# Kernel tuning notes

Measured on AMD Instinct MI355X. Metric: run time of the kernel, lower is better.

## Reference

```python
import jax, jax.numpy as jnp
import numpy as np

K = 8              # kernel_size
C_IN = 3           # input_channels
HID = 256          # hidden_state_size
MID = 256          # mid_layer_size
N_MAIN = 4         # num_main_layers
N_CLS = 1000       # num_classes
N_PIX = K * K      # num_pixel_values
IN_VEC = 2 + 1 + N_PIX * C_IN + HID   # 451
OUT_VEC = 2 + 1 + HID                 # 259
B, H, W = 128, 256, 256


def _lin_init(k, fan_in, fan_out):
    kw, kb = jax.random.split(k)
    bound = 1.0 / np.sqrt(fan_in)
    w = jax.random.uniform(kw, (fan_in, fan_out), jnp.float32, -bound, bound)
    b = jax.random.uniform(kb, (fan_out,), jnp.float32, -bound, bound)
    return w, b


def setup_inputs() -> dict:
    key = jax.random.key(0)
    ks = jax.random.split(key, 16)
    image = jax.random.normal(ks[0], (B, C_IN, H, W), jnp.float32)
    locations = jax.random.uniform(ks[1], (B, 2), jnp.float32)
    scales = jax.random.uniform(ks[2], (B, 1), jnp.float32)
    hidden_state = jax.random.normal(ks[3], (B, HID), jnp.float32)
    w0, b0 = _lin_init(ks[4], IN_VEC, MID)
    rws, rbs = [], []
    for i in range(N_MAIN):
        w, b = _lin_init(jax.random.fold_in(ks[5], i), MID, MID)
        rws.append(w); rbs.append(b)
    rw = jnp.stack(rws); rb = jnp.stack(rbs)          # [4,MID,MID], [4,MID]
    wf, bf = _lin_init(ks[6], MID, OUT_VEC)
    cw0, cb0 = _lin_init(ks[7], HID, MID)
    crw, crb = _lin_init(ks[8], MID, MID)
    cw1, cb1 = _lin_init(ks[9], MID, N_CLS)
    return {"image": image, "locations": locations, "scales": scales,
            "hidden_state": hidden_state, "w0": w0, "b0": b0, "rw": rw,
            "rb": rb, "wf": wf, "bf": bf, "cw0": cw0, "cb0": cb0,
            "crw": crw, "crb": crb, "cw1": cw1, "cb1": cb1}


def fourier_interp_2d(image, sample_points):
    """Band-limited (NUDFT) interpolation of image at continuous points.
    image: [B,C,H,W]; sample_points: [B,N,2] in normalized [0,1) (ij order).
    Returns [B,N,C]."""
    Bsz, C, Hh, Ww = image.shape
    F = jnp.fft.fft2(image)                       # [B,C,H,W] complex
    fy = jnp.fft.fftfreq(Hh) * Hh                 # integer freqs [H]
    fx = jnp.fft.fftfreq(Ww) * Ww                 # integer freqs [W]
    y = sample_points[..., 0]                     # [B,N]
    x = sample_points[..., 1]
    two_pi_i = 2j * jnp.pi
    Ey = jnp.exp(two_pi_i * y[..., None] * fy)    # [B,N,H]
    Ex = jnp.exp(two_pi_i * x[..., None] * fx)    # [B,N,W]
    tmp = jnp.einsum('bchw,bnh->bcnw', F, Ey)     # dominant compute
    vals = jnp.einsum('bcnw,bnw->bcn', tmp, Ex).real / (Hh * Ww)
    return jnp.transpose(vals, (0, 2, 1))         # [B,N,C]


def reference(image, locations, scales, hidden_state,
              w0, b0, rw, rb, wf, bf, cw0, cb0, crw, crb, cw1, cb1):
    Bsz = image.shape[0]
    # base meshgrid: [K,K,2], ij indexing, values arange(K)/K
    g = jnp.arange(K, dtype=image.dtype) / K
    mesh = jnp.stack(jnp.meshgrid(g, g, indexing='ij'), axis=-1)  # [K,K,2]
    coords = mesh[None] - locations[:, None, None, :]             # [B,K,K,2]
    coords = coords * scales[:, None, None, :]
    coords = coords.reshape(Bsz, N_PIX, 2)
    pix = fourier_interp_2d(image, coords)                        # [B,N,C]
    pix = pix.reshape(Bsz, N_PIX * C_IN)
    inp = jnp.concatenate([locations, scales, pix, hidden_state], axis=-1)
    h = inp @ w0 + b0
    for i in range(N_MAIN):
        h = jax.nn.relu(h @ rw[i] + rb[i] + h)
    out = jnp.tanh(h @ wf + bf)                                   # [B,OUT_VEC]
    new_loc = locations + out[:, :2]
    new_scale = scales + out[:, 2:3]
    new_hidden = hidden_state + out[:, 3:]
    c = jax.nn.relu(new_hidden @ cw0 + cb0)
    c = jax.nn.relu(c @ crw + crb + c)
    preds = jax.nn.softmax(c @ cw1 + cb1, axis=-1)
    # concat all outputs: [B, 2+1+HID+N_CLS]
    return jnp.concatenate([new_loc, new_scale, new_hidden, preds], axis=-1)
```

## Files before the change

### kernel.cpp

```cpp
#include <hip/hip_runtime.h>
#include <math.h>

#define BB 128
#define OUTROW 1259

typedef float vf4 __attribute__((ext_vector_type(4)));

__device__ __forceinline__ void dirichlet_ab(float t, float& A, float& Bv) {
    float r = t - rintf(t);
    float s256 = sinpif(256.0f * r);
    Bv = s256 * (1.0f / 256.0f);
    if (fabsf(r) < 1e-6f) {
        A = 1.0f;
    } else {
        float sp = sinpif(r), cp = cospif(r);
        A = Bv * cp / sp;
    }
}

__device__ __forceinline__ void warm_range(const float* __restrict__ p, int n4,
                                           int slot, int tid, float& s) {
    int per = (n4 + 255) / 256;
    int lo = slot * per;
    int hi = lo + per; if (hi > n4) hi = n4;
    for (int i = lo + tid; i < hi; i += 256) {
        const float4 v = *(const float4*)(p + 4 * (size_t)i);
        s += v.x + v.y + v.z + v.w;
    }
}

__global__ __launch_bounds__(256) void warm_kernel(
    const float* __restrict__ w0, const float* __restrict__ rw,
    const float* __restrict__ wf, const float* __restrict__ cw0,
    const float* __restrict__ crw, const float* __restrict__ cw1,
    float* __restrict__ sink)
{
    int slot = (int)(blockIdx.x >> 3);
    int tid = threadIdx.x;
    float s = 0.f;
    warm_range(w0,  28864, slot, tid, s);
    warm_range(rw,  65536, slot, tid, s);
    warm_range(wf,  16576, slot, tid, s);
    warm_range(cw0, 16384, slot, tid, s);
    warm_range(crw, 16384, slot, tid, s);
    warm_range(cw1, 64000, slot, tid, s);
    if (s == 1.0e30f) sink[0] = s;
}

__global__ __launch_bounds__(256) void interp_kernel(
    const float* __restrict__ image, const float* __restrict__ loc,
    const float* __restrict__ scl, float* __restrict__ pix)
{
    __shared__ float U[256 * 16];
    __shared__ float V[16 * 260];
    __shared__ float T[16 * 260];

    int bid = blockIdx.x;
    int b = bid / 3, c = bid % 3;
    int tid = threadIdx.x;
    float l0 = loc[2 * b], l1 = loc[2 * b + 1], sc = scl[b];

    {
        int p = tid;
        float tp = (float)p * (1.0f / 256.0f);
        #pragma unroll
        for (int iy = 0; iy < 8; ++iy) {
            float A, Bv;
            float y = ((float)iy * 0.125f - l0) * sc;
            dirichlet_ab(y - tp, A, Bv);
            int w = iy >> 1, o = iy & 1;
            U[p * 16 + w * 4 + o] = A;
            U[p * 16 + w * 4 + 2 + o] = Bv;
            float x = ((float)iy * 0.125f - l1) * sc;
            dirichlet_ab(x - tp, A, Bv);
            V[iy * 260 + p] = A;
            V[(8 + iy) * 260 + p] = Bv;
        }
    }
    __syncthreads();

    int wave = tid >> 6, lane = tid & 63;
    const float* img = image + (size_t)(b * 3 + c) * 65536 + lane * 4;

    float aA0[4] = {0, 0, 0, 0}, aA1[4] = {0, 0, 0, 0};
    float aB0[4] = {0, 0, 0, 0}, aB1[4] = {0, 0, 0, 0};
    #pragma unroll 4
    for (int p = 0; p < 256; ++p) {
        vf4 v = __builtin_nontemporal_load((const vf4*)(img + p * 256));
        const float4 u = *(const float4*)(&U[p * 16 + wave * 4]);
        aA0[0] += u.x * v[0]; aA0[1] += u.x * v[1]; aA0[2] += u.x * v[2]; aA0[3] += u.x * v[3];
        aA1[0] += u.y * v[0]; aA1[1] += u.y * v[1]; aA1[2] += u.y * v[2]; aA1[3] += u.y * v[3];
        aB0[0] += u.z * v[0]; aB0[1] += u.z * v[1]; aB0[2] += u.z * v[2]; aB0[3] += u.z * v[3];
        aB1[0] += u.w * v[0]; aB1[1] += u.w * v[1]; aB1[2] += u.w * v[2]; aB1[3] += u.w * v[3];
    }
    int iy0 = wave * 2;
    int q0 = lane * 4;
    #pragma unroll
    for (int j = 0; j < 4; ++j) {
        T[iy0 * 260 + q0 + j]       = aA0[j];
        T[(iy0 + 1) * 260 + q0 + j] = aA1[j];
        T[(8 + iy0) * 260 + q0 + j]     = aB0[j];
        T[(8 + iy0 + 1) * 260 + q0 + j] = aB1[j];
    }
    __syncthreads();

    int n = tid >> 2, sub = tid & 3;
    int iy = n >> 3, ix = n & 7;
    float s = 0.f;
    #pragma unroll 8
    for (int i = 0; i < 64; ++i) {
        int q = sub + 4 * i;
        s += T[iy * 260 + q] * V[ix * 260 + q] - T[(8 + iy) * 260 + q] * V[(8 + ix) * 260 + q];
    }
    s += __shfl_xor(s, 1);
    s += __shfl_xor(s, 2);
    if (sub == 0) pix[(b * 64 + n) * 3 + c] = s;
}

__global__ __launch_bounds__(1024, 1) void mlp_kernel(
    const float* __restrict__ loc, const float* __restrict__ scl,
    const float* __restrict__ hidden, const float* __restrict__ pix,
    const float* __restrict__ w0, const float* __restrict__ b0,
    const float* __restrict__ rw, const float* __restrict__ rb,
    const float* __restrict__ wf, const float* __restrict__ bf,
    const float* __restrict__ cw0, const float* __restrict__ cb0,
    const float* __restrict__ crw, const float* __restrict__ crb,
    const float* __restrict__ cw1, const float* __restrict__ cb1,
    float* __restrict__ out)
{
    __shared__ float s_in[452];
    __shared__ float s_h[256];
    __shared__ float s_o[260];
    __shared__ float s_part[8192];
    __shared__ float s_red[32];
    __shared__ float s_b0[256], s_rb[1024], s_bf[260], s_cb0[256], s_crb[256], s_cb1[1000];

    int b = blockIdx.x, tid = threadIdx.x;
    int jg = tid & 63, sub = tid >> 6;
    int j4 = jg * 4;
    float* orow = out + (size_t)b * OUTROW;

    if (tid < 2) s_in[tid] = loc[2 * b + tid];
    if (tid == 2) s_in[2] = scl[b];
    if (tid >= 256 && tid < 448) s_in[3 + (tid - 256)] = pix[b * 192 + (tid - 256)];
    if (tid >= 512 && tid < 768) s_in[195 + (tid - 512)] = hidden[b * 256 + (tid - 512)];
    if (tid < 256) s_b0[tid] = b0[tid];
    s_rb[tid] = rb[tid];
    if (tid < 259) s_bf[tid] = bf[tid];
    if (tid >= 256 && tid < 512) s_cb0[tid - 256] = cb0[tid - 256];
    if (tid >= 512 && tid < 768) s_crb[tid - 512] = crb[tid - 512];
    if (tid < 1000) s_cb1[tid] = cb1[tid];
    __syncthreads();

    {
        float4 acc = {0.f, 0.f, 0.f, 0.f};
        #pragma unroll
        for (int t = 0; t < 14; ++t) {
            int k = sub + 16 * t;
            float hv = s_in[k];
            float4 w = *(const float4*)(w0 + (size_t)k * 256 + j4);
            acc.x += hv * w.x; acc.y += hv * w.y; acc.z += hv * w.z; acc.w += hv * w.w;
        }
        #pragma unroll
        for (int t = 14; t < 28; ++t) {
            int k = sub + 16 * t;
            float hv = s_in[k];
            float4 w = *(const float4*)(w0 + (size_t)k * 256 + j4);
            acc.x += hv * w.x; acc.y += hv * w.y; acc.z += hv * w.z; acc.w += hv * w.w;
        }
        if (sub < 3) {
            int k = 448 + sub;
            float hv = s_in[k];
            float4 w = *(const float4*)(w0 + (size_t)k * 256 + j4);
            acc.x += hv * w.x; acc.y += hv * w.y; acc.z += hv * w.z; acc.w += hv * w.w;
        }
        *(float4*)(&s_part[sub * 256 + j4]) = acc;
    }
    __syncthreads();
    if (tid < 256) {
        float a = s_b0[tid];
        #pragma unroll
        for (int s = 0; s < 16; ++s) a += s_part[s * 256 + tid];
        s_h[tid] = a;
    }
    __syncthreads();

    #pragma unroll 1
    for (int L = 0; L < 4; ++L) {
        const float* W = rw + (size_t)L * 65536;
        float4 a = {0.f, 0.f, 0.f, 0.f};
        #pragma unroll
        for (int t = 0; t < 16; ++t) {
            int k = sub + 16 * t;
            float hv = s_h[k];
            float4 w = *(const float4*)(W + (size_t)k * 256 + j4);
            a.x += hv * w.x; a.y += hv * w.y; a.z += hv * w.z; a.w += hv * w.w;
        }
        *(float4*)(&s_part[sub * 256 + j4]) = a;
        __syncthreads();
        if (tid < 256) {
            float v = s_rb[L * 256 + tid] + s_h[tid];
            #pragma unroll
            for (int s = 0; s < 16; ++s) v += s_part[s * 256 + tid];
            s_h[tid] = fmaxf(v, 0.f);
        }
        __syncthreads();
    }

    {
        float a0 = 0.f, a1 = 0.f, a2 = 0.f, a3 = 0.f, e = 0.f;
        #pragma unroll 8
        for (int t = 0; t < 16; ++t) {
            int k = sub + 16 * t;
            float hv = s_h[k];
            const float* w = wf + (size_t)k * 259 + j4;
            a0 += hv * w[0]; a1 += hv * w[1]; a2 += hv * w[2]; a3 += hv * w[3];
            if (jg < 3) e += hv * wf[(size_t)k * 259 + 256 + jg];
        }
        s_part[sub * 260 + j4 + 0] = a0;
        s_part[sub * 260 + j4 + 1] = a1;
        s_part[sub * 260 + j4 + 2] = a2;
        s_part[sub * 260 + j4 + 3] = a3;
        if (jg < 3) s_part[sub * 260 + 256 + jg] = e;
    }
    __syncthreads();
    if (tid < 259) {
        float a = s_bf[tid];
        #pragma unroll
        for (int s = 0; s < 16; ++s) a += s_part[s * 260 + tid];
        s_o[tid] = tanhf(a);
    }
    __syncthreads();

    if (tid < 256) {
        float nh = s_in[195 + tid] + s_o[3 + tid];
        orow[3 + tid] = nh;
        s_h[tid] = nh;
    }
    if (tid == 256) orow[0] = s_in[0] + s_o[0];
    if (tid == 257) orow[1] = s_in[1] + s_o[1];
    if (tid == 258) orow[2] = s_in[2] + s_o[2];
    __syncthreads();

    {
        float4 a = {0.f, 0.f, 0.f, 0.f};
        #pragma unroll
        for (int t = 0; t < 16; ++t) {
            int k = sub + 16 * t;
            float hv = s_h[k];
            float4 w = *(const float4*)(cw0 + (size_t)k * 256 + j4);
            a.x += hv * w.x; a.y += hv * w.y; a.z += hv * w.z; a.w += hv * w.w;
        }
        *(float4*)(&s_part[sub * 256 + j4]) = a;
    }
    __syncthreads();
    if (tid < 256) {
        float v = s_cb0[tid];
        #pragma unroll
        for (int s = 0; s < 16; ++s) v += s_part[s * 256 + tid];
        s_h[tid] = fmaxf(v, 0.f);
    }
    __syncthreads();

    {
        float4 a = {0.f, 0.f, 0.f, 0.f};
        #pragma unroll
        for (int t = 0; t < 16; ++t) {
            int k = sub + 16 * t;
            float hv = s_h[k];
            float4 w = *(const float4*)(crw + (size_t)k * 256 + j4);
            a.x += hv * w.x; a.y += hv * w.y; a.z += hv * w.z; a.w += hv * w.w;
        }
        *(float4*)(&s_part[sub * 256 + j4]) = a;
        __syncthreads();
        if (tid < 256) {
            float v = s_crb[tid] + s_h[tid];
            #pragma unroll
            for (int s = 0; s < 16; ++s) v += s_part[s * 256 + tid];
            s_h[tid] = fmaxf(v, 0.f);
        }
        __syncthreads();
    }

    {
        int sub8 = tid >> 7, jg8 = tid & 127;
        int c4 = jg8 * 4;
        float4 acc0 = {0.f, 0.f, 0.f, 0.f};
        float4 acc1 = {0.f, 0.f, 0.f, 0.f};
        #pragma unroll 8
        for (int t = 0; t < 32; ++t) {
            int k = sub8 + 8 * t;
            float hv = s_h[k];
            const float* w = cw1 + (size_t)k * 1000;
            float4 wa = *(const float4*)(w + c4);
            acc0.x += hv * wa.x; acc0.y += hv * wa.y; acc0.z += hv * wa.z; acc0.w += hv * wa.w;
            if (jg8 < 122) {
                float4 wb = *(const float4*)(w + c4 + 512);
                acc1.x += hv * wb.x; acc1.y += hv * wb.y; acc1.z += hv * wb.z; acc1.w += hv * wb.w;
            }
        }
        *(float4*)(&s_part[sub8 * 1024 + c4]) = acc0;
        if (jg8 < 122) *(float4*)(&s_part[sub8 * 1024 + 512 + c4]) = acc1;
    }
    __syncthreads();

    float lgv = -1e30f;
    if (tid < 1000) {
        float a = s_cb1[tid];
        #pragma unroll
        for (int s = 0; s < 8; ++s) a += s_part[s * 1024 + tid];
        lgv = a;
    }

    int lane = tid & 63, wid = tid >> 6;
    float m = lgv;
    #pragma unroll
    for (int off = 1; off < 64; off <<= 1) m = fmaxf(m, __shfl_xor(m, off));
    if (lane == 0) s_red[wid] = m;
    __syncthreads();
    m = s_red[0];
    #pragma unroll
    for (int w = 1; w < 16; ++w) m = fmaxf(m, s_red[w]);

    float e = (tid < 1000) ? expf(lgv - m) : 0.f;
    float lsum = e;
    #pragma unroll
    for (int off = 1; off < 64; off <<= 1) lsum += __shfl_xor(lsum, off);
    if (lane == 0) s_red[16 + wid] = lsum;
    __syncthreads();
    float total = 0.f;
    #pragma unroll
    for (int w = 0; w < 16; ++w) total += s_red[16 + w];

    if (tid < 1000) orow[259 + tid] = e / total;
}

extern "C" void kernel_launch(void* const* d_in, const int* in_sizes, int n_in,
                              void* d_out, int out_size, void* d_ws, size_t ws_size,
                              hipStream_t stream) {
    const float* image  = (const float*)d_in[0];
    const float* loc    = (const float*)d_in[1];
    const float* scl    = (const float*)d_in[2];
    const float* hidden = (const float*)d_in[3];
    const float* w0  = (const float*)d_in[4];
    const float* b0  = (const float*)d_in[5];
    const float* rw  = (const float*)d_in[6];
    const float* rb  = (const float*)d_in[7];
    const float* wf  = (const float*)d_in[8];
    const float* bf  = (const float*)d_in[9];
    const float* cw0 = (const float*)d_in[10];
    const float* cb0 = (const float*)d_in[11];
    const float* crw = (const float*)d_in[12];
    const float* crb = (const float*)d_in[13];
    const float* cw1 = (const float*)d_in[14];
    const float* cb1 = (const float*)d_in[15];

    float* pix = (float*)d_ws;

    hipLaunchKernelGGL(warm_kernel, dim3(2048), dim3(256), 0, stream,
                       w0, rw, wf, cw0, crw, cw1, pix);
    hipLaunchKernelGGL(interp_kernel, dim3(BB * 3), dim3(256), 0, stream,
                       image, loc, scl, pix);
    hipLaunchKernelGGL(mlp_kernel, dim3(BB), dim3(1024), 0, stream,
                       loc, scl, hidden, pix,
                       w0, b0, rw, rb, wf, bf, cw0, cb0, crw, crb, cw1, cb1,
                       (float*)d_out);
}
```

Measured before the change: 86.98 us.

## Split classifier logits into separate wide kernel, drop cache-warm kernel, batch weight loads

Removes the weight-prefetch warm kernel. Moves the 256x1000 classifier GEMV out of the per-batch MLP kernel into a grid of 128x8 blocks, and adds a separate softmax kernel that reads logits back from the workspace. GEMV loops now issue all weight loads before the FMAs so more memory requests are in flight. The split buys more parallelism for the largest layer, but costs two extra launches and global round-trips. Dropping the warm kernel may also expose cold weight reads.

```diff
diff --git a/kernel.cpp b/kernel.cpp
--- a/kernel.cpp
+++ b/kernel.cpp
@@ -16,35 +16,6 @@
         float sp = sinpif(r), cp = cospif(r);
         A = Bv * cp / sp;
     }
-}
-
-__device__ __forceinline__ void warm_range(const float* __restrict__ p, int n4,
-                                           int slot, int tid, float& s) {
-    int per = (n4 + 255) / 256;
-    int lo = slot * per;
-    int hi = lo + per; if (hi > n4) hi = n4;
-    for (int i = lo + tid; i < hi; i += 256) {
-        const float4 v = *(const float4*)(p + 4 * (size_t)i);
-        s += v.x + v.y + v.z + v.w;
-    }
-}
-
-__global__ __launch_bounds__(256) void warm_kernel(
-    const float* __restrict__ w0, const float* __restrict__ rw,
-    const float* __restrict__ wf, const float* __restrict__ cw0,
-    const float* __restrict__ crw, const float* __restrict__ cw1,
-    float* __restrict__ sink)
-{
-    int slot = (int)(blockIdx.x >> 3);
-    int tid = threadIdx.x;
-    float s = 0.f;
-    warm_range(w0,  28864, slot, tid, s);
-    warm_range(rw,  65536, slot, tid, s);
-    warm_range(wf,  16576, slot, tid, s);
-    warm_range(cw0, 16384, slot, tid, s);
-    warm_range(crw, 16384, slot, tid, s);
-    warm_range(cw1, 64000, slot, tid, s);
-    if (s == 1.0e30f) sink[0] = s;
 }
 
 __global__ __launch_bounds__(256) void interp_kernel(
@@ -117,7 +88,29 @@
     if (sub == 0) pix[(b * 64 + n) * 3 + c] = s;
 }
 
-__global__ __launch_bounds__(1024, 1) void mlp_kernel(
+__device__ __forceinline__ void gemv256(const float* __restrict__ W,
+                                        const float* __restrict__ s_src,
+                                        float* __restrict__ s_part,
+                                        int sub, int j4)
+{
+    float4 wv[16];
+    float hv[16];
+    #pragma unroll
+    for (int t = 0; t < 16; ++t)
+        wv[t] = *(const float4*)(W + (size_t)(sub + 16 * t) * 256 + j4);
+    #pragma unroll
+    for (int t = 0; t < 16; ++t)
+        hv[t] = s_src[sub + 16 * t];
+    float4 a = {0.f, 0.f, 0.f, 0.f};
+    #pragma unroll
+    for (int t = 0; t < 16; ++t) {
+        a.x += hv[t] * wv[t].x; a.y += hv[t] * wv[t].y;
+        a.z += hv[t] * wv[t].z; a.w += hv[t] * wv[t].w;
+    }
+    *(float4*)(&s_part[sub * 256 + j4]) = a;
+}
+
+__global__ __launch_bounds__(1024, 1) void mlp_main(
     const float* __restrict__ loc, const float* __restrict__ scl,
     const float* __restrict__ hidden, const float* __restrict__ pix,
     const float* __restrict__ w0, const float* __restrict__ b0,
@@ -125,15 +118,14 @@
     const float* __restrict__ wf, const float* __restrict__ bf,
     const float* __restrict__ cw0, const float* __restrict__ cb0,
     const float* __restrict__ crw, const float* __restrict__ crb,
-    const float* __restrict__ cw1, const float* __restrict__ cb1,
-    float* __restrict__ out)
+    float* __restrict__ c1buf, float* __restrict__ out)
 {
     __shared__ float s_in[452];
     __shared__ float s_h[256];
+    __shared__ float s_c[256];
     __shared__ float s_o[260];
-    __shared__ float s_part[8192];
-    __shared__ float s_red[32];
-    __shared__ float s_b0[256], s_rb[1024], s_bf[260], s_cb0[256], s_crb[256], s_cb1[1000];
+    __shared__ float s_part[16 * 260];
+    __shared__ float s_b0[256], s_rb[1024], s_bf[260], s_cb0[256], s_crb[256];
 
     int b = blockIdx.x, tid = threadIdx.x;
     int jg = tid & 63, sub = tid >> 6;
@@ -149,24 +141,35 @@
     if (tid < 259) s_bf[tid] = bf[tid];
     if (tid >= 256 && tid < 512) s_cb0[tid - 256] = cb0[tid - 256];
     if (tid >= 512 && tid < 768) s_crb[tid - 512] = crb[tid - 512];
-    if (tid < 1000) s_cb1[tid] = cb1[tid];
     __syncthreads();
 
     {
         float4 acc = {0.f, 0.f, 0.f, 0.f};
-        #pragma unroll
-        for (int t = 0; t < 14; ++t) {
-            int k = sub + 16 * t;
-            float hv = s_in[k];
-            float4 w = *(const float4*)(w0 + (size_t)k * 256 + j4);
-            acc.x += hv * w.x; acc.y += hv * w.y; acc.z += hv * w.z; acc.w += hv * w.w;
-        }
-        #pragma unroll
-        for (int t = 14; t < 28; ++t) {
-            int k = sub + 16 * t;
-            float hv = s_in[k];
-            float4 w = *(const float4*)(w0 + (size_t)k * 256 + j4);
-            acc.x += hv * w.x; acc.y += hv * w.y; acc.z += hv * w.z; acc.w += hv * w.w;
+        {
+            float4 wv[14]; float hv[14];
+            #pragma unroll
+            for (int t = 0; t < 14; ++t)
+                wv[t] = *(const float4*)(w0 + (size_t)(sub + 16 * t) * 256 + j4);
+            #pragma unroll
+            for (int t = 0; t < 14; ++t) hv[t] = s_in[sub + 16 * t];
+            #pragma unroll
+            for (int t = 0; t < 14; ++t) {
+                acc.x += hv[t] * wv[t].x; acc.y += hv[t] * wv[t].y;
+                acc.z += hv[t] * wv[t].z; acc.w += hv[t] * wv[t].w;
+            }
+        }
+        {
+            float4 wv[14]; float hv[14];
+            #pragma unroll
+            for (int t = 0; t < 14; ++t)
+                wv[t] = *(const float4*)(w0 + (size_t)(sub + 16 * (t + 14)) * 256 + j4);
+            #pragma unroll
+            for (int t = 0; t < 14; ++t) hv[t] = s_in[sub + 16 * (t + 14)];
+            #pragma unroll
+            for (int t = 0; t < 14; ++t) {
+                acc.x += hv[t] * wv[t].x; acc.y += hv[t] * wv[t].y;
+                acc.z += hv[t] * wv[t].z; acc.w += hv[t] * wv[t].w;
+            }
         }
         if (sub < 3) {
             int k = 448 + sub;
@@ -187,16 +190,7 @@
 
     #pragma unroll 1
     for (int L = 0; L < 4; ++L) {
-        const float* W = rw + (size_t)L * 65536;
-        float4 a = {0.f, 0.f, 0.f, 0.f};
-        #pragma unroll
-        for (int t = 0; t < 16; ++t) {
-            int k = sub + 16 * t;
-            float hv = s_h[k];
-            float4 w = *(const float4*)(W + (size_t)k * 256 + j4);
-            a.x += hv * w.x; a.y += hv * w.y; a.z += hv * w.z; a.w += hv * w.w;
-        }
-        *(float4*)(&s_part[sub * 256 + j4]) = a;
+        gemv256(rw + (size_t)L * 65536, s_h, s_part, sub, j4);
         __syncthreads();
         if (tid < 256) {
             float v = s_rb[L * 256 + tid] + s_h[tid];
@@ -242,75 +236,78 @@
     if (tid == 258) orow[2] = s_in[2] + s_o[2];
     __syncthreads();
 
-    {
-        float4 a = {0.f, 0.f, 0.f, 0.f};
-        #pragma unroll
-        for (int t = 0; t < 16; ++t) {
-            int k = sub + 16 * t;
-            float hv = s_h[k];
-            float4 w = *(const float4*)(cw0 + (size_t)k * 256 + j4);
-            a.x += hv * w.x; a.y += hv * w.y; a.z += hv * w.z; a.w += hv * w.w;
-        }
-        *(float4*)(&s_part[sub * 256 + j4]) = a;
-    }
+    gemv256(cw0, s_h, s_part, sub, j4);
     __syncthreads();
     if (tid < 256) {
         float v = s_cb0[tid];
         #pragma unroll
         for (int s = 0; s < 16; ++s) v += s_part[s * 256 + tid];
-        s_h[tid] = fmaxf(v, 0.f);
-    }
-    __syncthreads();
-
-    {
-        float4 a = {0.f, 0.f, 0.f, 0.f};
-        #pragma unroll
-        for (int t = 0; t < 16; ++t) {
-            int k = sub + 16 * t;
-            float hv = s_h[k];
-            float4 w = *(const float4*)(crw + (size_t)k * 256 + j4);
-            a.x += hv * w.x; a.y += hv * w.y; a.z += hv * w.z; a.w += hv * w.w;
-        }
-        *(float4*)(&s_part[sub * 256 + j4]) = a;
-        __syncthreads();
-        if (tid < 256) {
-            float v = s_crb[tid] + s_h[tid];
-            #pragma unroll
-            for (int s = 0; s < 16; ++s) v += s_part[s * 256 + tid];
-            s_h[tid] = fmaxf(v, 0.f);
-        }
-        __syncthreads();
-    }
-
-    {
-        int sub8 = tid >> 7, jg8 = tid & 127;
-        int c4 = jg8 * 4;
-        float4 acc0 = {0.f, 0.f, 0.f, 0.f};
-        float4 acc1 = {0.f, 0.f, 0.f, 0.f};
-        #pragma unroll 8
-        for (int t = 0; t < 32; ++t) {
-            int k = sub8 + 8 * t;
-            float hv = s_h[k];
-            const float* w = cw1 + (size_t)k * 1000;
-            float4 wa = *(const float4*)(w + c4);
-            acc0.x += hv * wa.x; acc0.y += hv * wa.y; acc0.z += hv * wa.z; acc0.w += hv * wa.w;
-            if (jg8 < 122) {
-                float4 wb = *(const float4*)(w + c4 + 512);
-                acc1.x += hv * wb.x; acc1.y += hv * wb.y; acc1.z += hv * wb.z; acc1.w += hv * wb.w;
-            }
-        }
-        *(float4*)(&s_part[sub8 * 1024 + c4]) = acc0;
-        if (jg8 < 122) *(float4*)(&s_part[sub8 * 1024 + 512 + c4]) = acc1;
-    }
-    __syncthreads();
-
-    float lgv = -1e30f;
-    if (tid < 1000) {
-        float a = s_cb1[tid];
-        #pragma unroll
-        for (int s = 0; s < 8; ++s) a += s_part[s * 1024 + tid];
-        lgv = a;
-    }
+        s_c[tid] = fmaxf(v, 0.f);
+    }
+    __syncthreads();
+
+    gemv256(crw, s_c, s_part, sub, j4);
+    __syncthreads();
+    if (tid < 256) {
+        float v = s_crb[tid] + s_c[tid];
+        #pragma unroll
+        for (int s = 0; s < 16; ++s) v += s_part[s * 256 + tid];
+        c1buf[b * 256 + tid] = fmaxf(v, 0.f);
+    }
+}
+
+__global__ __launch_bounds__(1024, 1) void logits_kernel(
+    const float* __restrict__ c1buf, const float* __restrict__ cw1,
+    const float* __restrict__ cb1, float* __restrict__ logits)
+{
+    __shared__ float s_c1[256];
+    __shared__ float s_part[32 * 128];
+
+    int b = blockIdx.x, s = blockIdx.y, tid = threadIdx.x;
+    if (tid < 256) s_c1[tid] = c1buf[b * 256 + tid];
+    __syncthreads();
+
+    int cg = tid & 31, sub = tid >> 5;
+    int c4 = cg * 4;
+    int col0 = s * 128 + c4;
+    bool valid = (col0 + 3) < 1000;
+
+    float4 acc = {0.f, 0.f, 0.f, 0.f};
+    if (valid) {
+        float4 wv[8]; float hv[8];
+        #pragma unroll
+        for (int t = 0; t < 8; ++t)
+            wv[t] = *(const float4*)(cw1 + (size_t)(sub + 32 * t) * 1000 + col0);
+        #pragma unroll
+        for (int t = 0; t < 8; ++t) hv[t] = s_c1[sub + 32 * t];
+        #pragma unroll
+        for (int t = 0; t < 8; ++t) {
+            acc.x += hv[t] * wv[t].x; acc.y += hv[t] * wv[t].y;
+            acc.z += hv[t] * wv[t].z; acc.w += hv[t] * wv[t].w;
+        }
+    }
+    *(float4*)(&s_part[sub * 128 + c4]) = acc;
+    __syncthreads();
+
+    if (tid < 128) {
+        int col = s * 128 + tid;
+        if (col < 1000) {
+            float a = cb1[col];
+            #pragma unroll
+            for (int ss = 0; ss < 32; ++ss) a += s_part[ss * 128 + tid];
+            logits[(size_t)b * 1000 + col] = a;
+        }
+    }
+}
+
+__global__ __launch_bounds__(1024) void softmax_kernel(
+    const float* __restrict__ logits, float* __restrict__ out)
+{
+    __shared__ float s_red[32];
+    int b = blockIdx.x, tid = threadIdx.x;
+    float* orow = out + (size_t)b * OUTROW;
+
+    float lgv = (tid < 1000) ? logits[(size_t)b * 1000 + tid] : -1e30f;
 
     int lane = tid & 63, wid = tid >> 6;
     float m = lgv;
@@ -355,14 +352,19 @@
     const float* cw1 = (const float*)d_in[14];
     const float* cb1 = (const float*)d_in[15];
 
-    float* pix = (float*)d_ws;
-
-    hipLaunchKernelGGL(warm_kernel, dim3(2048), dim3(256), 0, stream,
-                       w0, rw, wf, cw0, crw, cw1, pix);
+    float* ws     = (float*)d_ws;
+    float* pix    = ws;
+    float* c1buf  = ws + 24576;
+    float* logits = ws + 24576 + 32768;
+
     hipLaunchKernelGGL(interp_kernel, dim3(BB * 3), dim3(256), 0, stream,
                        image, loc, scl, pix);
-    hipLaunchKernelGGL(mlp_kernel, dim3(BB), dim3(1024), 0, stream,
+    hipLaunchKernelGGL(mlp_main, dim3(BB), dim3(1024), 0, stream,
                        loc, scl, hidden, pix,
-                       w0, b0, rw, rb, wf, bf, cw0, cb0, crw, crb, cw1, cb1,
-                       (float*)d_out);
-}
+                       w0, b0, rw, rb, wf, bf, cw0, cb0, crw, crb,
+                       c1buf, (float*)d_out);
+    hipLaunchKernelGGL(logits_kernel, dim3(BB, 8), dim3(1024), 0, stream,
+                       c1buf, cw1, cb1, logits);
+    hipLaunchKernelGGL(softmax_kernel, dim3(BB), dim3(1024), 0, stream,
+                       logits, (float*)d_out);
+}
```

New measurement: 85.52 us. Within noise of the previous version (-1.7%).
